# Kernel tuning notes

Hardware: AMD Instinct MI355X
Metric: run time of the kernel (lower is better)

Reference implementation:

```python
import jax, jax.numpy as jnp
import numpy as np

NP_, B_ = 44, 400000

def setup_inputs() -> dict:
    key = jax.random.key(0)
    k_x, k1, k2, k3, k4 = jax.random.split(key, 5)
    return {
        "X": jax.random.normal(k_x, (NP_, 1, B_), dtype=jnp.float32),
        "lin1s": jax.random.normal(k1, (NP_, 4, 1), dtype=jnp.float32),
        "lin2s": jax.random.normal(k2, (NP_, 8, 4), dtype=jnp.float32),
        "lin3s": jax.random.normal(k3, (NP_, 4, 8), dtype=jnp.float32),
        "lin4s": jax.random.normal(k4, (NP_, 1, 4), dtype=jnp.float32),
    }

def reference(X, lin1s, lin2s, lin3s, lin4s):
    # forward_all: chained batched tiny GEMMs with ReLU, 'lik,lkj->lij'
    h = jax.nn.relu(jnp.einsum('lik,lkj->lij', lin1s, X))   # (NP, 4, B)
    h = jax.nn.relu(jnp.einsum('lik,lkj->lij', lin2s, h))   # (NP, 8, B)
    h = jax.nn.relu(jnp.einsum('lik,lkj->lij', lin3s, h))   # (NP, 4, B)
    return jnp.einsum('lik,lkj->lij', lin4s, h)             # (NP, 1, B)
```

## Files before the change

kernel.cpp:

```cpp
#include <hip/hip_runtime.h>

#define NP  44
#define B   400000
#define B4  (B / 4)
#define BLK 256
#define CPT 4

typedef float v2f __attribute__((ext_vector_type(2)));

__device__ __forceinline__ v2f relu2(v2f a) {
    return __builtin_elementwise_max(a, (v2f)0.0f);
}

__device__ __forceinline__ v2f mlp_pair(
    const float w1[4], const float w2[8][4],
    const float w3[4][8], const float w4[4], v2f x)
{
#pragma clang fp contract(fast)
    v2f h1[4];
#pragma unroll
    for (int i = 0; i < 4; ++i) h1[i] = relu2(w1[i] * x);

    v2f h2[8];
#pragma unroll
    for (int i = 0; i < 8; ++i) {
        v2f a = w2[i][0] * h1[0];
#pragma unroll
        for (int k = 1; k < 4; ++k) a += w2[i][k] * h1[k];
        h2[i] = relu2(a);
    }

    v2f h3[4];
#pragma unroll
    for (int i = 0; i < 4; ++i) {
        v2f a = w3[i][0] * h2[0];
#pragma unroll
        for (int k = 1; k < 8; ++k) a += w3[i][k] * h2[k];
        h3[i] = relu2(a);
    }

    v2f a = w4[0] * h3[0];
#pragma unroll
    for (int k = 1; k < 4; ++k) a += w4[k] * h3[k];
    return a;
}

__global__ __launch_bounds__(BLK) void fused_mlp_kernel(
    const float* __restrict__ X,
    const float* __restrict__ W1,
    const float* __restrict__ W2,
    const float* __restrict__ W3,
    const float* __restrict__ W4,
    float* __restrict__ out)
{
    const int l    = blockIdx.y;
    const int base = blockIdx.x * (BLK * CPT) + threadIdx.x;

    const float* p1 = W1 + l * 4;
    const float* p2 = W2 + l * 32;
    const float* p3 = W3 + l * 32;
    const float* p4 = W4 + l * 4;

    float w1[4], w2[8][4], w3[4][8], w4[4];
#pragma unroll
    for (int i = 0; i < 4; ++i) w1[i] = p1[i];
#pragma unroll
    for (int i = 0; i < 8; ++i)
#pragma unroll
        for (int k = 0; k < 4; ++k) w2[i][k] = p2[i * 4 + k];
#pragma unroll
    for (int i = 0; i < 4; ++i)
#pragma unroll
        for (int k = 0; k < 8; ++k) w3[i][k] = p3[i * 8 + k];
#pragma unroll
    for (int i = 0; i < 4; ++i) w4[i] = p4[i];

    const float4* Xp = (const float4*)(X + (size_t)l * B);
    float4*       Op = (float4*)(out + (size_t)l * B);

    if ((blockIdx.x + 1) * (BLK * CPT) <= B4) {
        float4 xv[CPT];
#pragma unroll
        for (int c = 0; c < CPT; ++c) xv[c] = Xp[base + c * BLK];

        float4 rv[CPT];
#pragma unroll
        for (int c = 0; c < CPT; ++c) {
            v2f p0 = {xv[c].x, xv[c].y};
            v2f p1v = {xv[c].z, xv[c].w};
            v2f r0 = mlp_pair(w1, w2, w3, w4, p0);
            v2f r1 = mlp_pair(w1, w2, w3, w4, p1v);
            rv[c] = make_float4(r0.x, r0.y, r1.x, r1.y);
        }
#pragma unroll
        for (int c = 0; c < CPT; ++c) Op[base + c * BLK] = rv[c];
    } else {
#pragma unroll
        for (int c = 0; c < CPT; ++c) {
            const int idx = base + c * BLK;
            if (idx < B4) {
                float4 xv = Xp[idx];
                v2f p0 = {xv.x, xv.y};
                v2f p1v = {xv.z, xv.w};
                v2f r0 = mlp_pair(w1, w2, w3, w4, p0);
                v2f r1 = mlp_pair(w1, w2, w3, w4, p1v);
                Op[idx] = make_float4(r0.x, r0.y, r1.x, r1.y);
            }
        }
    }
}

extern "C" void kernel_launch(void* const* d_in, const int* in_sizes, int n_in,
                              void* d_out, int out_size, void* d_ws, size_t ws_size,
                              hipStream_t stream) {
    const float* X  = (const float*)d_in[0];
    const float* W1 = (const float*)d_in[1];
    const float* W2 = (const float*)d_in[2];
    const float* W3 = (const float*)d_in[3];
    const float* W4 = (const float*)d_in[4];
    float* out = (float*)d_out;

    dim3 grid((B4 + BLK * CPT - 1) / (BLK * CPT), NP);
    fused_mlp_kernel<<<grid, BLK, 0, stream>>>(X, W1, W2, W3, W4, out);
}
```

Measured before the change: 147.8 us.

## Collapse scalar-input ReLU MLP into piecewise-linear gain per plane

Uses positive homogeneity of the ReLU network with a single scalar input. Each block precomputes two gains, one for positive inputs and one for negative inputs, by propagating the weights. Each element then needs only one multiply and select instead of the full chain of tiny GEMMs. This turns the kernel from ALU-bound into bandwidth-bound, at the cost of redundant per-block weight collapsing and different floating-point rounding order.

```diff
diff --git a/kernel.cpp b/kernel.cpp
--- a/kernel.cpp
+++ b/kernel.cpp
@@ -6,46 +6,56 @@
 #define BLK 256
 #define CPT 4
 
-typedef float v2f __attribute__((ext_vector_type(2)));
+__device__ __forceinline__ void collapse_weights(
+    const float* __restrict__ p1, const float* __restrict__ p2,
+    const float* __restrict__ p3, const float* __restrict__ p4,
+    float& gp, float& gn)
+{
+    float w1p[4], w1n[4];
+#pragma unroll
+    for (int k = 0; k < 4; ++k) {
+        float w = p1[k];
+        w1p[k] = fmaxf(w, 0.0f);
+        w1n[k] = fminf(w, 0.0f);
+    }
 
-__device__ __forceinline__ v2f relu2(v2f a) {
-    return __builtin_elementwise_max(a, (v2f)0.0f);
+    float d2p[8], d2n[8];
+#pragma unroll
+    for (int i = 0; i < 8; ++i) {
+        float ap = 0.0f, an = 0.0f;
+#pragma unroll
+        for (int k = 0; k < 4; ++k) {
+            float w = p2[i * 4 + k];
+            ap = fmaf(w, w1p[k], ap);
+            an = fmaf(w, w1n[k], an);
+        }
+        d2p[i] = fmaxf(ap, 0.0f);
+        d2n[i] = fminf(an, 0.0f);
+    }
+
+    float f3p[4], f3n[4];
+#pragma unroll
+    for (int j = 0; j < 4; ++j) {
+        float ap = 0.0f, an = 0.0f;
+#pragma unroll
+        for (int i = 0; i < 8; ++i) {
+            float w = p3[j * 8 + i];
+            ap = fmaf(w, d2p[i], ap);
+            an = fmaf(w, d2n[i], an);
+        }
+        f3p[j] = fmaxf(ap, 0.0f);
+        f3n[j] = fminf(an, 0.0f);
+    }
+
+    gp = 0.0f; gn = 0.0f;
+#pragma unroll
+    for (int j = 0; j < 4; ++j) {
+        gp = fmaf(p4[j], f3p[j], gp);
+        gn = fmaf(p4[j], f3n[j], gn);
+    }
 }
 
-__device__ __forceinline__ v2f mlp_pair(
-    const float w1[4], const float w2[8][4],
-    const float w3[4][8], const float w4[4], v2f x)
-{
-#pragma clang fp contract(fast)
-    v2f h1[4];
-#pragma unroll
-    for (int i = 0; i < 4; ++i) h1[i] = relu2(w1[i] * x);
-
-    v2f h2[8];
-#pragma unroll
-    for (int i = 0; i < 8; ++i) {
-        v2f a = w2[i][0] * h1[0];
-#pragma unroll
-        for (int k = 1; k < 4; ++k) a += w2[i][k] * h1[k];
-        h2[i] = relu2(a);
-    }
-
-    v2f h3[4];
-#pragma unroll
-    for (int i = 0; i < 4; ++i) {
-        v2f a = w3[i][0] * h2[0];
-#pragma unroll
-        for (int k = 1; k < 8; ++k) a += w3[i][k] * h2[k];
-        h3[i] = relu2(a);
-    }
-
-    v2f a = w4[0] * h3[0];
-#pragma unroll
-    for (int k = 1; k < 4; ++k) a += w4[k] * h3[k];
-    return a;
-}
-
-__global__ __launch_bounds__(BLK) void fused_mlp_kernel(
+__global__ __launch_bounds__(BLK) void collapsed_mlp_kernel(
     const float* __restrict__ X,
     const float* __restrict__ W1,
     const float* __restrict__ W2,
@@ -56,55 +66,43 @@
     const int l    = blockIdx.y;
     const int base = blockIdx.x * (BLK * CPT) + threadIdx.x;
 
-    const float* p1 = W1 + l * 4;
-    const float* p2 = W2 + l * 32;
-    const float* p3 = W3 + l * 32;
-    const float* p4 = W4 + l * 4;
-
-    float w1[4], w2[8][4], w3[4][8], w4[4];
-#pragma unroll
-    for (int i = 0; i < 4; ++i) w1[i] = p1[i];
-#pragma unroll
-    for (int i = 0; i < 8; ++i)
-#pragma unroll
-        for (int k = 0; k < 4; ++k) w2[i][k] = p2[i * 4 + k];
-#pragma unroll
-    for (int i = 0; i < 4; ++i)
-#pragma unroll
-        for (int k = 0; k < 8; ++k) w3[i][k] = p3[i * 8 + k];
-#pragma unroll
-    for (int i = 0; i < 4; ++i) w4[i] = p4[i];
-
     const float4* Xp = (const float4*)(X + (size_t)l * B);
     float4*       Op = (float4*)(out + (size_t)l * B);
 
-    if ((blockIdx.x + 1) * (BLK * CPT) <= B4) {
-        float4 xv[CPT];
+    const bool full = (blockIdx.x + 1) * (BLK * CPT) <= B4;
+
+    float4 xv[CPT];
+    if (full) {
 #pragma unroll
         for (int c = 0; c < CPT; ++c) xv[c] = Xp[base + c * BLK];
+    }
 
-        float4 rv[CPT];
+    float gp, gn;
+    collapse_weights(W1 + l * 4, W2 + l * 32, W3 + l * 32, W4 + l * 4, gp, gn);
+
+    if (full) {
 #pragma unroll
         for (int c = 0; c < CPT; ++c) {
-            v2f p0 = {xv[c].x, xv[c].y};
-            v2f p1v = {xv[c].z, xv[c].w};
-            v2f r0 = mlp_pair(w1, w2, w3, w4, p0);
-            v2f r1 = mlp_pair(w1, w2, w3, w4, p1v);
-            rv[c] = make_float4(r0.x, r0.y, r1.x, r1.y);
+            float4 v = xv[c];
+            float4 r;
+            r.x = v.x * (v.x >= 0.0f ? gp : gn);
+            r.y = v.y * (v.y >= 0.0f ? gp : gn);
+            r.z = v.z * (v.z >= 0.0f ? gp : gn);
+            r.w = v.w * (v.w >= 0.0f ? gp : gn);
+            Op[base + c * BLK] = r;
         }
-#pragma unroll
-        for (int c = 0; c < CPT; ++c) Op[base + c * BLK] = rv[c];
     } else {
 #pragma unroll
         for (int c = 0; c < CPT; ++c) {
             const int idx = base + c * BLK;
             if (idx < B4) {
-                float4 xv = Xp[idx];
-                v2f p0 = {xv.x, xv.y};
-                v2f p1v = {xv.z, xv.w};
-                v2f r0 = mlp_pair(w1, w2, w3, w4, p0);
-                v2f r1 = mlp_pair(w1, w2, w3, w4, p1v);
-                Op[idx] = make_float4(r0.x, r0.y, r1.x, r1.y);
+                float4 v = Xp[idx];
+                float4 r;
+                r.x = v.x * (v.x >= 0.0f ? gp : gn);
+                r.y = v.y * (v.y >= 0.0f ? gp : gn);
+                r.z = v.z * (v.z >= 0.0f ? gp : gn);
+                r.w = v.w * (v.w >= 0.0f ? gp : gn);
+                Op[idx] = r;
             }
         }
     }
@@ -121,5 +119,5 @@
     float* out = (float*)d_out;
 
     dim3 grid((B4 + BLK * CPT - 1) / (BLK * CPT), NP);
-    fused_mlp_kernel<<<grid, BLK, 0, stream>>>(X, W1, W2, W3, W4, out);
+    collapsed_mlp_kernel<<<grid, BLK, 0, stream>>>(X, W1, W2, W3, W4, out);
 }
```

After: 127.1 us. 1.16x faster.
